# Optimization experiments

Measured on AMD Instinct MI355X. Metric: run time of the kernel, lower is better.

## Reference

```python
import jax, jax.numpy as jnp
import numpy as np

N = 100_000      # nodes
E = 3_200_000    # edges (avg degree 32)
IN = 128         # in_dim
H = 64           # hidden
C = 2            # n_classes
G = 128          # graphs in batch


def setup_inputs() -> dict:
    key = jax.random.key(0)
    ks = jax.random.split(key, 14)
    x = jax.random.normal(ks[0], (N, IN), jnp.float32)
    edge_index = jax.random.randint(ks[1], (2, E), 0, N)
    edge_weight = jax.random.uniform(ks[2], (E,), jnp.float32)
    # deterministic sorted batch assignment -> every graph non-empty
    batch = (jnp.arange(N) * G) // N
    def lin(k, fi, fo):
        s = 1.0 / np.sqrt(fi)
        return jax.random.uniform(k, (fi, fo), jnp.float32, -s, s)
    return {
        "x": x, "edge_index": edge_index, "edge_weight": edge_weight,
        "batch": batch, "n_graphs": G,
        "W1": lin(ks[3], IN, H), "b1": jnp.zeros((H,), jnp.float32),
        "W2": lin(ks[4], H, H),  "b2": jnp.zeros((H,), jnp.float32),
        "pw": lin(ks[5], H, 1),  "pb": jnp.zeros((1,), jnp.float32),
        "lw1": lin(ks[6], 2 * H, H), "lb1": jnp.zeros((H,), jnp.float32),
        "lw2": lin(ks[7], H, C),     "lb2": jnp.zeros((C,), jnp.float32),
    }


def _gcn(x, edge_index, edge_weight, W, b):
    # PyG GCNConv with add_self_loops=False:
    # out = D^{-1/2} A D^{-1/2} (x W) + b, messages flow row->col
    h = x @ W                                   # [N, H]
    row, col = edge_index[0], edge_index[1]
    n = x.shape[0]
    deg = jax.ops.segment_sum(edge_weight, col, num_segments=n)
    dis = jnp.where(deg > 0, jax.lax.rsqrt(jnp.maximum(deg, 1e-12)), 0.0)
    norm = dis[row] * edge_weight * dis[col]    # [E]
    msg = h[row] * norm[:, None]                # [E, H] gather + scale
    out = jax.ops.segment_sum(msg, col, num_segments=n)  # scatter-add
    return out + b


def reference(x, edge_index, edge_weight, batch, n_graphs,
              W1, b1, W2, b2, pw, pb, lw1, lb1, lw2, lb2):
    h = jax.nn.relu(_gcn(x, edge_index, edge_weight, W1, b1))
    h = jax.nn.relu(_gcn(h, edge_index, edge_weight, W2, b2))
    # TopoPool (stand-in): learned per-node score gating (see notes)
    score = jax.nn.sigmoid(h @ pw + pb)         # [N, 1]
    h = h * score
    # global max pool || global mean pool per graph
    gmx = jax.ops.segment_max(h, batch, num_segments=n_graphs)
    gsum = jax.ops.segment_sum(h, batch, num_segments=n_graphs)
    cnt = jax.ops.segment_sum(jnp.ones((h.shape[0], 1), h.dtype), batch,
                              num_segments=n_graphs)
    gmean = gsum / jnp.maximum(cnt, 1.0)
    g = jnp.concatenate([gmx, gmean], axis=1)   # [G, 2H]
    g = jax.nn.relu(g @ lw1 + lb1)
    return g @ lw2 + lb2                        # [G, C]
```

## Files before the change

### kernel.cpp

```cpp
#include <hip/hip_runtime.h>
#include <math.h>


#define TPN_BLK 256
#define P1_EPT  16
#define P1_CHUNK (TPN_BLK * P1_EPT)
#define NB_MAX  512
#define BCAP    12288
#define CSH     13
#define NKEY    4096

__global__ __launch_bounds__(256)
void tpn_bin(const int* __restrict__ ei, const float* __restrict__ ew,
             int* __restrict__ binCur, uint2* __restrict__ binned,
             int E, int NB) {
    __shared__ uint2          sbuf[P1_CHUNK];
    __shared__ unsigned short sbin[P1_CHUNK];
    __shared__ int hist[NB_MAX];
    __shared__ int loff[NB_MAX];
    __shared__ int lrank[NB_MAX];
    __shared__ int gbase[NB_MAX];
    __shared__ int ssc[256];

    int tid = threadIdx.x;
    for (int b = tid; b < NB_MAX; b += 256) { hist[b] = 0; lrank[b] = 0; }
    __syncthreads();

    int base = blockIdx.x * P1_CHUNK;
    uint2 ed[P1_EPT];
    int   bn[P1_EPT];
    #pragma unroll
    for (int j = 0; j < P1_EPT; ++j) {
        int e = base + tid + j * 256;
        bn[j] = -1;
        if (e < E) {
            int r = ei[e], c = ei[E + e];
            bn[j] = c >> 8;
            ed[j] = make_uint2((unsigned)r | ((unsigned)(c & 255) << 17),
                               __float_as_uint(ew[e]));
            atomicAdd(&hist[bn[j]], 1);
        }
    }
    __syncthreads();
    {
        int b0 = 2 * tid, b1 = 2 * tid + 1;
        int h0 = hist[b0], h1 = hist[b1];
        int s = h0 + h1;
        ssc[tid] = s;
        __syncthreads();
        for (int st = 1; st < 256; st <<= 1) {
            int v = (tid >= st) ? ssc[tid - st] : 0;
            __syncthreads();
            ssc[tid] += v;
            __syncthreads();
        }
        int pre = ssc[tid] - s;
        loff[b0] = pre;
        loff[b1] = pre + h0;
    }
    __syncthreads();
    for (int b = tid; b < NB; b += 256) {
        int h = hist[b];
        if (h > 0) gbase[b] = atomicAdd(&binCur[b], h);
    }
    #pragma unroll
    for (int j = 0; j < P1_EPT; ++j) {
        if (bn[j] >= 0) {
            int p = loff[bn[j]] + atomicAdd(&lrank[bn[j]], 1);
            sbuf[p] = ed[j];
            sbin[p] = (unsigned short)bn[j];
        }
    }
    __syncthreads();
    int m = min(E - base, P1_CHUNK);
    for (int i = tid; i < m; i += 256) {
        uint2 u = sbuf[i];
        int b = sbin[i];
        int dst = gbase[b] + (i - loff[b]);
        if (dst < BCAP) binned[(size_t)b * BCAP + dst] = u;
    }
}

__global__ void tpn_binscan(const int* __restrict__ binCur, int* __restrict__ binOff,
                            int NB) {
    __shared__ int sh[NB_MAX];
    int t = threadIdx.x;
    int v = (t < NB) ? min(binCur[t], BCAP) : 0;
    sh[t] = v;
    __syncthreads();
    for (int st = 1; st < NB_MAX; st <<= 1) {
        int u = (t >= st) ? sh[t - st] : 0;
        __syncthreads();
        sh[t] += u;
        __syncthreads();
    }
    if (t < NB) binOff[t] = sh[t] - v;
}

__global__ __launch_bounds__(256)
void tpn_build(const uint2* __restrict__ binned, const int* __restrict__ binCur,
               const int* __restrict__ binOff, uint2* __restrict__ packed,
               int* __restrict__ off, int* __restrict__ cnt,
               float* __restrict__ dis, int N) {
    __shared__ int   kcnt[NKEY];
    __shared__ int   koff[NKEY];
    __shared__ int   krank[NKEY];
    __shared__ float ldeg[256];
    __shared__ int   lcnt[256];
    __shared__ int   ssc[256];
    int b = blockIdx.x, tid = threadIdx.x;
    int m = min(binCur[b], BCAP);
    const uint2* src = binned + (size_t)b * BCAP;
    for (int i = tid; i < NKEY; i += 256) { kcnt[i] = 0; krank[i] = 0; }
    ldeg[tid] = 0.0f; lcnt[tid] = 0;
    __syncthreads();
    for (int i = tid; i < m; i += 256) {
        uint2 u = src[i];
        int ln = u.x >> 17;
        int ch = (u.x & 0x1FFFF) >> CSH;
        atomicAdd(&kcnt[(ln << 4) | ch], 1);
        atomicAdd(&ldeg[ln], __uint_as_float(u.y));
        atomicAdd(&lcnt[ln], 1);
    }
    __syncthreads();
    {
        int base16 = tid << 4;
        int loc[16]; int s = 0;
        #pragma unroll
        for (int i = 0; i < 16; ++i) { loc[i] = s; s += kcnt[base16 + i]; }
        ssc[tid] = s;
        __syncthreads();
        for (int st = 1; st < 256; st <<= 1) {
            int v = (tid >= st) ? ssc[tid - st] : 0;
            __syncthreads();
            ssc[tid] += v;
            __syncthreads();
        }
        int pre = ssc[tid] - s;
        #pragma unroll
        for (int i = 0; i < 16; ++i) koff[base16 + i] = pre + loc[i];
    }
    __syncthreads();
    {
        int node = (b << 8) + tid;
        if (node < N) {
            off[node] = binOff[b] + koff[tid << 4];
            cnt[node] = lcnt[tid];
            float s = ldeg[tid];
            dis[node] = (s > 0.0f) ? rsqrtf(fmaxf(s, 1e-12f)) : 0.0f;
        }
    }
    int gb = binOff[b];
    for (int i = tid; i < m; i += 256) {
        uint2 u = src[i];
        int ln = u.x >> 17;
        int ch = (u.x & 0x1FFFF) >> CSH;
        int k = (ln << 4) | ch;
        int rk = atomicAdd(&krank[k], 1);
        packed[gb + koff[k] + rk] = make_uint2(u.x & 0x1FFFF, u.y);
    }
}

__global__ __launch_bounds__(256, 4)
void tpn_gemm_t(const float* __restrict__ X, const float* __restrict__ W,
                const float* __restrict__ dis, float* __restrict__ Y,
                int N, int K) {
    __shared__ float sX[64][68];
    __shared__ float sW[64][64];
    const int t  = threadIdx.x;
    const int r  = t >> 4;
    const int cc = t & 15;
    const int fg = t & 15;
    const int ng = t >> 4;
    const int nb = blockIdx.x * 64;

    float acc[4][4] = {{0.f}};

    for (int kc = 0; kc < K; kc += 64) {
        __syncthreads();
        #pragma unroll
        for (int p = 0; p < 4; ++p) {
            int n = nb + r + p * 16;
            int ns = (n < N) ? n : (N - 1);
            float4 v = *reinterpret_cast<const float4*>(X + (size_t)ns * K + kc + 4 * cc);
            *reinterpret_cast<float4*>(&sX[r + p * 16][4 * cc]) = v;
        }
        #pragma unroll
        for (int p = 0; p < 4; ++p) {
            int k = kc + r + p * 16;
            float4 v = *reinterpret_cast<const float4*>(W + (size_t)k * 64 + 4 * cc);
            *reinterpret_cast<float4*>(&sW[r + p * 16][4 * cc]) = v;
        }
        __syncthreads();
        #pragma unroll 4
        for (int k = 0; k < 64; ++k) {
            float4 wv = *reinterpret_cast<const float4*>(&sW[k][4 * fg]);
            float x0 = sX[4 * ng + 0][k];
            float x1 = sX[4 * ng + 1][k];
            float x2 = sX[4 * ng + 2][k];
            float x3 = sX[4 * ng + 3][k];
            acc[0][0] = fmaf(x0, wv.x, acc[0][0]);
            acc[0][1] = fmaf(x0, wv.y, acc[0][1]);
            acc[0][2] = fmaf(x0, wv.z, acc[0][2]);
            acc[0][3] = fmaf(x0, wv.w, acc[0][3]);
            acc[1][0] = fmaf(x1, wv.x, acc[1][0]);
            acc[1][1] = fmaf(x1, wv.y, acc[1][1]);
            acc[1][2] = fmaf(x1, wv.z, acc[1][2]);
            acc[1][3] = fmaf(x1, wv.w, acc[1][3]);
            acc[2][0] = fmaf(x2, wv.x, acc[2][0]);
            acc[2][1] = fmaf(x2, wv.y, acc[2][1]);
            acc[2][2] = fmaf(x2, wv.z, acc[2][2]);
            acc[2][3] = fmaf(x2, wv.w, acc[2][3]);
            acc[3][0] = fmaf(x3, wv.x, acc[3][0]);
            acc[3][1] = fmaf(x3, wv.y, acc[3][1]);
            acc[3][2] = fmaf(x3, wv.z, acc[3][2]);
            acc[3][3] = fmaf(x3, wv.w, acc[3][3]);
        }
    }
    #pragma unroll
    for (int i = 0; i < 4; ++i) {
        int n = nb + 4 * ng + i;
        if (n < N) {
            float d = dis[n];
            float4 v = make_float4(acc[i][0] * d, acc[i][1] * d,
                                   acc[i][2] * d, acc[i][3] * d);
            *reinterpret_cast<float4*>(Y + (size_t)n * 64 + 4 * fg) = v;
        }
    }
}

template <bool FUSE_SCORE>
__global__ __launch_bounds__(256)
void tpn_agg(const uint2* __restrict__ packed, const int* __restrict__ off,
             const int* __restrict__ cnt, const float* __restrict__ dis,
             const float* __restrict__ Hin, const float* __restrict__ bias,
             const float* __restrict__ pw, const float* __restrict__ pb,
             float* __restrict__ Hout, int N) {
    int wid = (blockIdx.x * blockDim.x + threadIdx.x) >> 6;
    int lane = threadIdx.x & 63;
    if (wid >= N) return;
    const int eg = lane >> 4;
    const int fb = (lane & 15) * 4;
    int start = off[wid], n = cnt[wid];
    const uint2* b = packed + start;
    const float* hp = Hin + fb;

    float4 A0 = {0.f, 0.f, 0.f, 0.f};
    float4 A1 = {0.f, 0.f, 0.f, 0.f};
    int j = 0;
    for (; j + 8 <= n; j += 8) {
        uint2 p0 = b[j + eg];
        uint2 p1 = b[j + 4 + eg];
        float4 v0 = *reinterpret_cast<const float4*>(hp + (size_t)p0.x * 64);
        float4 v1 = *reinterpret_cast<const float4*>(hp + (size_t)p1.x * 64);
        float w0 = __uint_as_float(p0.y);
        float w1 = __uint_as_float(p1.y);
        A0.x = fmaf(w0, v0.x, A0.x); A0.y = fmaf(w0, v0.y, A0.y);
        A0.z = fmaf(w0, v0.z, A0.z); A0.w = fmaf(w0, v0.w, A0.w);
        A1.x = fmaf(w1, v1.x, A1.x); A1.y = fmaf(w1, v1.y, A1.y);
        A1.z = fmaf(w1, v1.z, A1.z); A1.w = fmaf(w1, v1.w, A1.w);
    }
    for (; j < n; j += 4) {
        int idx = j + eg;
        uint2 p = (idx < n) ? b[idx] : make_uint2(0u, 0u);
        float4 v = *reinterpret_cast<const float4*>(hp + (size_t)p.x * 64);
        float w = __uint_as_float(p.y);
        A0.x = fmaf(w, v.x, A0.x); A0.y = fmaf(w, v.y, A0.y);
        A0.z = fmaf(w, v.z, A0.z); A0.w = fmaf(w, v.w, A0.w);
    }
    float4 acc;
    acc.x = A0.x + A1.x; acc.y = A0.y + A1.y;
    acc.z = A0.z + A1.z; acc.w = A0.w + A1.w;
    acc.x += __shfl_xor(acc.x, 16); acc.x += __shfl_xor(acc.x, 32);
    acc.y += __shfl_xor(acc.y, 16); acc.y += __shfl_xor(acc.y, 32);
    acc.z += __shfl_xor(acc.z, 16); acc.z += __shfl_xor(acc.z, 32);
    acc.w += __shfl_xor(acc.w, 16); acc.w += __shfl_xor(acc.w, 32);

    float dc = dis[wid];
    const float4 bv = *reinterpret_cast<const float4*>(bias + fb);
    float4 h;
    h.x = fmaxf(fmaf(acc.x, dc, bv.x), 0.0f);
    h.y = fmaxf(fmaf(acc.y, dc, bv.y), 0.0f);
    h.z = fmaxf(fmaf(acc.z, dc, bv.z), 0.0f);
    h.w = fmaxf(fmaf(acc.w, dc, bv.w), 0.0f);
    if (FUSE_SCORE) {
        const float4 pv = *reinterpret_cast<const float4*>(pw + fb);
        float t = h.x * pv.x + h.y * pv.y + h.z * pv.z + h.w * pv.w;
        #pragma unroll
        for (int m = 1; m <= 8; m <<= 1) t += __shfl_xor(t, m);
        float s = 1.0f / (1.0f + expf(-(t + pb[0])));
        h.x *= s; h.y *= s; h.z *= s; h.w *= s;
    }
    if (eg == 0)
        *reinterpret_cast<float4*>(Hout + (size_t)wid * 64 + fb) = h;
}

__global__ void tpn_pool(const float* __restrict__ Hs, const int* __restrict__ batch,
                         int N, float* __restrict__ Gf) {
    int g = blockIdx.x;
    int s, e;
    {
        int lo = 0, hi = N;
        while (lo < hi) { int mid = (lo + hi) >> 1; if (batch[mid] < g) lo = mid + 1; else hi = mid; }
        s = lo;
        lo = 0; hi = N;
        while (lo < hi) { int mid = (lo + hi) >> 1; if (batch[mid] < g + 1) lo = mid + 1; else hi = mid; }
        e = lo;
    }
    int lane = threadIdx.x & 63;
    int w = threadIdx.x >> 6;
    float mx = -3.4e38f, sm = 0.0f;
    for (int i = s + w; i < e; i += 4) {
        float v = Hs[(size_t)i * 64 + lane];
        mx = fmaxf(mx, v);
        sm += v;
    }
    __shared__ float shm[4][64], shs[4][64];
    shm[w][lane] = mx; shs[w][lane] = sm;
    __syncthreads();
    if (w == 0) {
        mx = fmaxf(fmaxf(shm[0][lane], shm[1][lane]), fmaxf(shm[2][lane], shm[3][lane]));
        sm = shs[0][lane] + shs[1][lane] + shs[2][lane] + shs[3][lane];
        float c = (float)(e - s);
        float inv = 1.0f / fmaxf(c, 1.0f);
        Gf[g * 128 + lane]      = mx;
        Gf[g * 128 + 64 + lane] = sm * inv;
    }
}

__global__ void tpn_mlp(const float* __restrict__ Gf, const float* __restrict__ lw1,
                        const float* __restrict__ lb1, const float* __restrict__ lw2,
                        const float* __restrict__ lb2, float* __restrict__ out,
                        int G, int C) {
    int wid = (blockIdx.x * blockDim.x + threadIdx.x) >> 6;
    int lane = threadIdx.x & 63;
    if (wid >= G) return;
    const float* gr = Gf + (size_t)wid * 128;
    float acc = lb1[lane];
    for (int k = 0; k < 128; k += 4) {
        float4 gv = *reinterpret_cast<const float4*>(gr + k);
        acc = fmaf(gv.x, lw1[(k + 0) * 64 + lane], acc);
        acc = fmaf(gv.y, lw1[(k + 1) * 64 + lane], acc);
        acc = fmaf(gv.z, lw1[(k + 2) * 64 + lane], acc);
        acc = fmaf(gv.w, lw1[(k + 3) * 64 + lane], acc);
    }
    float t = fmaxf(acc, 0.0f);
    for (int c = 0; c < C; ++c) {
        float v = t * lw2[lane * C + c];
        #pragma unroll
        for (int m = 32; m > 0; m >>= 1) v += __shfl_xor(v, m);
        if (lane == 0) out[wid * C + c] = v + lb2[c];
    }
}

extern "C" void kernel_launch(void* const* d_in, const int* in_sizes, int n_in,
                              void* d_out, int out_size, void* d_ws, size_t ws_size,
                              hipStream_t stream) {
    const float* x   = (const float*)d_in[0];
    const int*   ei  = (const int*)  d_in[1];
    const float* ew  = (const float*)d_in[2];
    const int*   bat = (const int*)  d_in[3];
    const float* W1  = (const float*)d_in[5];
    const float* b1  = (const float*)d_in[6];
    const float* W2  = (const float*)d_in[7];
    const float* b2  = (const float*)d_in[8];
    const float* pw  = (const float*)d_in[9];
    const float* pb  = (const float*)d_in[10];
    const float* lw1 = (const float*)d_in[11];
    const float* lb1 = (const float*)d_in[12];
    const float* lw2 = (const float*)d_in[13];
    const float* lb2 = (const float*)d_in[14];
    float* out = (float*)d_out;

    const int N  = in_sizes[3];
    const int E  = in_sizes[2];
    const int IN = in_sizes[0] / N;
    const int C  = in_sizes[14];
    const int G  = out_size / C;
    const int NB = (N + 255) >> 8;

    char* ws = (char*)d_ws;
    size_t o = 0;
    auto alloc = [&](size_t bytes) { void* p = ws + o; o = (o + bytes + 255) & ~(size_t)255; return p; };
    int*   off    = (int*)  alloc((size_t)N * 4);
    int*   cnt    = (int*)  alloc((size_t)N * 4);
    float* dis    = (float*)alloc((size_t)N * 4);
    int*   binCur = (int*)  alloc((size_t)NB_MAX * 4);
    int*   binOff = (int*)  alloc((size_t)NB_MAX * 4);
    float* Gf     = (float*)alloc((size_t)G * 128 * 4);
    uint2* packed = (uint2*)alloc((size_t)E * 8);
    float* hA     = (float*)alloc((size_t)N * 64 * 4);
    float* hB     = (float*)alloc((size_t)N * 64 * 4);
    uint2* binned = (uint2*)hA;
    (void)n_in; (void)ws_size;

    (void)hipMemsetAsync(binCur, 0, (size_t)NB_MAX * 4, stream);

    const int p1b   = (E + P1_CHUNK - 1) / P1_CHUNK;
    const int ggrid = (N + 63) / 64;
    const int agrid = (N * 64 + TPN_BLK - 1) / TPN_BLK;

    tpn_bin<<<p1b, TPN_BLK, 0, stream>>>(ei, ew, binCur, binned, E, NB);
    tpn_binscan<<<1, NB_MAX, 0, stream>>>(binCur, binOff, NB);
    tpn_build<<<NB, 256, 0, stream>>>(binned, binCur, binOff, packed, off, cnt, dis, N);

    tpn_gemm_t<<<ggrid, 256, 0, stream>>>(x, W1, dis, hA, N, IN);
    tpn_agg<false><<<agrid, TPN_BLK, 0, stream>>>(packed, off, cnt, dis, hA, b1, pw, pb, hB, N);

    tpn_gemm_t<<<ggrid, 256, 0, stream>>>(hB, W2, dis, hA, N, 64);
    tpn_agg<true><<<agrid, TPN_BLK, 0, stream>>>(packed, off, cnt, dis, hA, b2, pw, pb, hB, N);

    tpn_pool<<<G, TPN_BLK, 0, stream>>>(hB, bat, N, Gf);
    tpn_mlp<<<(G * 64 + TPN_BLK - 1) / TPN_BLK, TPN_BLK, 0, stream>>>(Gf, lw1, lb1, lw2, lb2, out, G, C);
}
```

Baseline: 424.2 us.

## Chunk aggregation by source-node range with grid barriers for cache locality

The build kernel now writes a chunk-major offset table (16 source-node chunks per destination node) in place of per-node offset and count arrays. The aggregation kernel gives each wave 32 destination nodes and walks the source chunks in order, with a software grid barrier between chunks so all blocks gather from the same slice of H (about 2 MB) together. The goal is to keep gathered rows resident in L2 and cut random-gather traffic. The cost is less edge-level parallelism: each 16-lane group walks one node's edges one at a time with dependent loads. There are also 12 spin barriers per launch, whose correctness relies on all blocks being co-resident.

```diff
diff --git a/kernel.cpp b/kernel.cpp
--- a/kernel.cpp
+++ b/kernel.cpp
@@ -100,19 +100,18 @@
 __global__ __launch_bounds__(256)
 void tpn_build(const uint2* __restrict__ binned, const int* __restrict__ binCur,
                const int* __restrict__ binOff, uint2* __restrict__ packed,
-               int* __restrict__ off, int* __restrict__ cnt,
-               float* __restrict__ dis, int N) {
+               int* __restrict__ offcm, float* __restrict__ dis,
+               int N, int Ntot) {
     __shared__ int   kcnt[NKEY];
     __shared__ int   koff[NKEY];
     __shared__ int   krank[NKEY];
     __shared__ float ldeg[256];
-    __shared__ int   lcnt[256];
     __shared__ int   ssc[256];
     int b = blockIdx.x, tid = threadIdx.x;
     int m = min(binCur[b], BCAP);
     const uint2* src = binned + (size_t)b * BCAP;
     for (int i = tid; i < NKEY; i += 256) { kcnt[i] = 0; krank[i] = 0; }
-    ldeg[tid] = 0.0f; lcnt[tid] = 0;
+    ldeg[tid] = 0.0f;
     __syncthreads();
     for (int i = tid; i < m; i += 256) {
         uint2 u = src[i];
@@ -120,7 +119,6 @@
         int ch = (u.x & 0x1FFFF) >> CSH;
         atomicAdd(&kcnt[(ln << 4) | ch], 1);
         atomicAdd(&ldeg[ln], __uint_as_float(u.y));
-        atomicAdd(&lcnt[ln], 1);
     }
     __syncthreads();
     {
@@ -144,13 +142,15 @@
     {
         int node = (b << 8) + tid;
         if (node < N) {
-            off[node] = binOff[b] + koff[tid << 4];
-            cnt[node] = lcnt[tid];
             float s = ldeg[tid];
             dis[node] = (s > 0.0f) ? rsqrtf(fmaxf(s, 1e-12f)) : 0.0f;
         }
     }
     int gb = binOff[b];
+    for (int k = tid; k < NKEY; k += 256) {
+        int ln = k >> 4, ch = k & 15;
+        offcm[(size_t)ch * Ntot + (b << 8) + ln] = gb + koff[k];
+    }
     for (int i = tid; i < m; i += 256) {
         uint2 u = src[i];
         int ln = u.x >> 17;
@@ -230,69 +230,77 @@
 }
 
 template <bool FUSE_SCORE>
-__global__ __launch_bounds__(256)
-void tpn_agg(const uint2* __restrict__ packed, const int* __restrict__ off,
-             const int* __restrict__ cnt, const float* __restrict__ dis,
-             const float* __restrict__ Hin, const float* __restrict__ bias,
-             const float* __restrict__ pw, const float* __restrict__ pb,
-             float* __restrict__ Hout, int N) {
-    int wid = (blockIdx.x * blockDim.x + threadIdx.x) >> 6;
-    int lane = threadIdx.x & 63;
-    if (wid >= N) return;
-    const int eg = lane >> 4;
-    const int fb = (lane & 15) * 4;
-    int start = off[wid], n = cnt[wid];
-    const uint2* b = packed + start;
+__global__ __launch_bounds__(256, 4)
+void tpn_aggc(const uint2* __restrict__ packed, const int* __restrict__ offcm,
+              const float* __restrict__ dis, const float* __restrict__ Hin,
+              const float* __restrict__ bias, const float* __restrict__ pw,
+              const float* __restrict__ pb, float* __restrict__ Hout,
+              int N, int Ntot, int NCH, int* __restrict__ bar, int nblk) {
+    const int tid  = threadIdx.x;
+    const int wid  = blockIdx.x * 4 + (tid >> 6);
+    const int lane = tid & 63;
+    const int l32  = lane & 31;
+    const int g    = lane >> 4;
+    const int fb   = (lane & 15) * 4;
+    const int nodeBase = wid * 32;
     const float* hp = Hin + fb;
 
-    float4 A0 = {0.f, 0.f, 0.f, 0.f};
-    float4 A1 = {0.f, 0.f, 0.f, 0.f};
-    int j = 0;
-    for (; j + 8 <= n; j += 8) {
-        uint2 p0 = b[j + eg];
-        uint2 p1 = b[j + 4 + eg];
-        float4 v0 = *reinterpret_cast<const float4*>(hp + (size_t)p0.x * 64);
-        float4 v1 = *reinterpret_cast<const float4*>(hp + (size_t)p1.x * 64);
-        float w0 = __uint_as_float(p0.y);
-        float w1 = __uint_as_float(p1.y);
-        A0.x = fmaf(w0, v0.x, A0.x); A0.y = fmaf(w0, v0.y, A0.y);
-        A0.z = fmaf(w0, v0.z, A0.z); A0.w = fmaf(w0, v0.w, A0.w);
-        A1.x = fmaf(w1, v1.x, A1.x); A1.y = fmaf(w1, v1.y, A1.y);
-        A1.z = fmaf(w1, v1.z, A1.z); A1.w = fmaf(w1, v1.w, A1.w);
-    }
-    for (; j < n; j += 4) {
-        int idx = j + eg;
-        uint2 p = (idx < n) ? b[idx] : make_uint2(0u, 0u);
-        float4 v = *reinterpret_cast<const float4*>(hp + (size_t)p.x * 64);
-        float w = __uint_as_float(p.y);
-        A0.x = fmaf(w, v.x, A0.x); A0.y = fmaf(w, v.y, A0.y);
-        A0.z = fmaf(w, v.z, A0.z); A0.w = fmaf(w, v.w, A0.w);
-    }
-    float4 acc;
-    acc.x = A0.x + A1.x; acc.y = A0.y + A1.y;
-    acc.z = A0.z + A1.z; acc.w = A0.w + A1.w;
-    acc.x += __shfl_xor(acc.x, 16); acc.x += __shfl_xor(acc.x, 32);
-    acc.y += __shfl_xor(acc.y, 16); acc.y += __shfl_xor(acc.y, 32);
-    acc.z += __shfl_xor(acc.z, 16); acc.z += __shfl_xor(acc.z, 32);
-    acc.w += __shfl_xor(acc.w, 16); acc.w += __shfl_xor(acc.w, 32);
-
-    float dc = dis[wid];
+    float4 a[8];
+    #pragma unroll
+    for (int t = 0; t < 8; ++t) a[t] = make_float4(0.f, 0.f, 0.f, 0.f);
+
+    for (int c = 0; c < NCH; ++c) {
+        int sv = offcm[(size_t)c * Ntot + nodeBase + l32];
+        int ev = offcm[(size_t)(c + 1) * Ntot + nodeBase + l32];
+        #pragma unroll
+        for (int t = 0; t < 8; ++t) {
+            int js = __shfl(sv, 4 * t + g);
+            int je = __shfl(ev, 4 * t + g);
+            for (int j = js; j < je; ++j) {
+                uint2 p = packed[j];
+                float w = __uint_as_float(p.y);
+                float4 v = *reinterpret_cast<const float4*>(hp + (size_t)p.x * 64);
+                a[t].x = fmaf(w, v.x, a[t].x);
+                a[t].y = fmaf(w, v.y, a[t].y);
+                a[t].z = fmaf(w, v.z, a[t].z);
+                a[t].w = fmaf(w, v.w, a[t].w);
+            }
+        }
+        if (c + 1 < NCH) {
+            __syncthreads();
+            if (tid == 0) {
+                atomicAdd(&bar[c], 1);
+                int sp = 0;
+                while (atomicAdd(&bar[c], 0) < nblk && ++sp < 256)
+                    __builtin_amdgcn_s_sleep(8);
+            }
+            __syncthreads();
+        }
+    }
+
     const float4 bv = *reinterpret_cast<const float4*>(bias + fb);
-    float4 h;
-    h.x = fmaxf(fmaf(acc.x, dc, bv.x), 0.0f);
-    h.y = fmaxf(fmaf(acc.y, dc, bv.y), 0.0f);
-    h.z = fmaxf(fmaf(acc.z, dc, bv.z), 0.0f);
-    h.w = fmaxf(fmaf(acc.w, dc, bv.w), 0.0f);
-    if (FUSE_SCORE) {
-        const float4 pv = *reinterpret_cast<const float4*>(pw + fb);
-        float t = h.x * pv.x + h.y * pv.y + h.z * pv.z + h.w * pv.w;
-        #pragma unroll
-        for (int m = 1; m <= 8; m <<= 1) t += __shfl_xor(t, m);
-        float s = 1.0f / (1.0f + expf(-(t + pb[0])));
-        h.x *= s; h.y *= s; h.z *= s; h.w *= s;
-    }
-    if (eg == 0)
-        *reinterpret_cast<float4*>(Hout + (size_t)wid * 64 + fb) = h;
+    float4 pv = make_float4(0.f, 0.f, 0.f, 0.f);
+    if (FUSE_SCORE) pv = *reinterpret_cast<const float4*>(pw + fb);
+    #pragma unroll
+    for (int t = 0; t < 8; ++t) {
+        int node = nodeBase + 4 * t + g;
+        if (node < N) {
+            float d = dis[node];
+            float4 h;
+            h.x = fmaxf(fmaf(a[t].x, d, bv.x), 0.f);
+            h.y = fmaxf(fmaf(a[t].y, d, bv.y), 0.f);
+            h.z = fmaxf(fmaf(a[t].z, d, bv.z), 0.f);
+            h.w = fmaxf(fmaf(a[t].w, d, bv.w), 0.f);
+            if (FUSE_SCORE) {
+                float s = h.x * pv.x + h.y * pv.y + h.z * pv.z + h.w * pv.w;
+                #pragma unroll
+                for (int m2 = 1; m2 <= 8; m2 <<= 1) s += __shfl_xor(s, m2);
+                float sg = 1.0f / (1.0f + expf(-(s + pb[0])));
+                h.x *= sg; h.y *= sg; h.z *= sg; h.w *= sg;
+            }
+            *reinterpret_cast<float4*>(Hout + (size_t)node * 64 + fb) = h;
+        }
+    }
 }
 
 __global__ void tpn_pool(const float* __restrict__ Hs, const int* __restrict__ batch,
@@ -372,43 +380,47 @@
     const float* lb2 = (const float*)d_in[14];
     float* out = (float*)d_out;
 
-    const int N  = in_sizes[3];
-    const int E  = in_sizes[2];
-    const int IN = in_sizes[0] / N;
-    const int C  = in_sizes[14];
-    const int G  = out_size / C;
-    const int NB = (N + 255) >> 8;
+    const int N    = in_sizes[3];
+    const int E    = in_sizes[2];
+    const int IN   = in_sizes[0] / N;
+    const int C    = in_sizes[14];
+    const int G    = out_size / C;
+    const int NB   = (N + 255) >> 8;
+    const int Ntot = NB << 8;
+    const int NCH  = (Ntot + (1 << CSH) - 1) >> CSH;
 
     char* ws = (char*)d_ws;
     size_t o = 0;
     auto alloc = [&](size_t bytes) { void* p = ws + o; o = (o + bytes + 255) & ~(size_t)255; return p; };
-    int*   off    = (int*)  alloc((size_t)N * 4);
-    int*   cnt    = (int*)  alloc((size_t)N * 4);
     float* dis    = (float*)alloc((size_t)N * 4);
     int*   binCur = (int*)  alloc((size_t)NB_MAX * 4);
+    int*   bar    = (int*)  alloc((size_t)64 * 4);
     int*   binOff = (int*)  alloc((size_t)NB_MAX * 4);
     float* Gf     = (float*)alloc((size_t)G * 128 * 4);
+    int*   offcm  = (int*)  alloc((size_t)16 * Ntot * 4);
     uint2* packed = (uint2*)alloc((size_t)E * 8);
     float* hA     = (float*)alloc((size_t)N * 64 * 4);
     float* hB     = (float*)alloc((size_t)N * 64 * 4);
     uint2* binned = (uint2*)hA;
     (void)n_in; (void)ws_size;
 
-    (void)hipMemsetAsync(binCur, 0, (size_t)NB_MAX * 4, stream);
+    (void)hipMemsetAsync(binCur, 0, (size_t)(NB_MAX + 64) * 4 + 256, stream);
 
     const int p1b   = (E + P1_CHUNK - 1) / P1_CHUNK;
     const int ggrid = (N + 63) / 64;
-    const int agrid = (N * 64 + TPN_BLK - 1) / TPN_BLK;
+    const int ablk  = Ntot / 128;
 
     tpn_bin<<<p1b, TPN_BLK, 0, stream>>>(ei, ew, binCur, binned, E, NB);
     tpn_binscan<<<1, NB_MAX, 0, stream>>>(binCur, binOff, NB);
-    tpn_build<<<NB, 256, 0, stream>>>(binned, binCur, binOff, packed, off, cnt, dis, N);
+    tpn_build<<<NB, 256, 0, stream>>>(binned, binCur, binOff, packed, offcm, dis, N, Ntot);
 
     tpn_gemm_t<<<ggrid, 256, 0, stream>>>(x, W1, dis, hA, N, IN);
-    tpn_agg<false><<<agrid, TPN_BLK, 0, stream>>>(packed, off, cnt, dis, hA, b1, pw, pb, hB, N);
+    tpn_aggc<false><<<ablk, 256, 0, stream>>>(packed, offcm, dis, hA, b1, pw, pb, hB,
+                                              N, Ntot, NCH, bar, ablk);
 
     tpn_gemm_t<<<ggrid, 256, 0, stream>>>(hB, W2, dis, hA, N, 64);
-    tpn_agg<true><<<agrid, TPN_BLK, 0, stream>>>(packed, off, cnt, dis, hA, b2, pw, pb, hB, N);
+    tpn_aggc<true><<<ablk, 256, 0, stream>>>(packed, offcm, dis, hA, b2, pw, pb, hB,
+                                             N, Ntot, NCH, bar + 16, ablk);
 
     tpn_pool<<<G, TPN_BLK, 0, stream>>>(hB, bat, N, Gf);
     tpn_mlp<<<(G * 64 + TPN_BLK - 1) / TPN_BLK, TPN_BLK, 0, stream>>>(Gf, lw1, lb1, lw2, lb2, out, G, C);
```

Measured after the change: 1.691 ms. +298.6%, slower.
